# Kernel tuning notes

Hardware: AMD Instinct MI355X
Metric: run time of the kernel (lower is better)

The kernel has to match this reference:

```python
import jax, jax.numpy as jnp
import numpy as np

B, S, D = 4, 2048, 1024
H, E = 16, 64  # n_heads, head_size; H*E == D


def setup_inputs() -> dict:
    key = jax.random.key(0)
    ks = jax.random.split(key, 6)
    sd = 1.0 / np.sqrt(D)
    x = jax.random.normal(ks[0], (B, S, D), dtype=jnp.float32)
    # per-head Q/K/V projection weights, stacked: [H, D, E]
    Wq = jax.random.uniform(ks[1], (H, D, E), jnp.float32, -sd, sd)
    Wk = jax.random.uniform(ks[2], (H, D, E), jnp.float32, -sd, sd)
    Wv = jax.random.uniform(ks[3], (H, D, E), jnp.float32, -sd, sd)
    Wp = jax.random.uniform(ks[4], (D, D), jnp.float32, -sd, sd)
    bp = jax.random.uniform(ks[5], (D,), jnp.float32, -sd, sd)
    return {"x": x, "Wq": Wq, "Wk": Wk, "Wv": Wv, "Wp": Wp, "bp": bp}


def reference(x, Wq, Wk, Wv, Wp, bp):
    # Per-head projections (all heads batched): [B, H, S, E]
    q = jnp.einsum('bsd,hde->bhse', x, Wq)
    k = jnp.einsum('bsd,hde->bhse', x, Wk)
    v = jnp.einsum('bsd,hde->bhse', x, Wv)
    scale = E ** -0.5
    # Full causal score matrix [B, H, S, S]
    wei = jnp.einsum('bhse,bhte->bhst', q, k) * scale
    causal = jnp.tril(jnp.ones((S, S), dtype=bool))
    wei = jnp.where(causal, wei, -jnp.inf)
    wei = jax.nn.softmax(wei, axis=-1)
    out = jnp.einsum('bhst,bhte->bhse', wei, v)
    # concat heads along feature dim: [B, S, H*E]
    out = out.transpose(0, 2, 1, 3).reshape(B, S, H * E)
    # output projection (dropout is identity in eval)
    return out @ Wp.T + bp
```

## Files before the change

kernel.cpp:

```cpp
#include <hip/hip_runtime.h>

#define B_ 4
#define S_ 2048
#define D_ 1024
#define H_ 16
#define E_ 64
#define M_ (B_*S_)

typedef __attribute__((ext_vector_type(8))) short short8;
typedef __attribute__((ext_vector_type(4))) float floatx4;

#define GLD16(g, l) __builtin_amdgcn_global_load_lds( \
    (const __attribute__((address_space(1))) unsigned*)(g), \
    (__attribute__((address_space(3))) unsigned*)(l), 16, 0, 0)

__device__ __forceinline__ ushort f2b(float f) {
    union { float f; unsigned u; } v; v.f = f;
    unsigned r = v.u + 0x7fffu + ((v.u >> 16) & 1u);
    return (ushort)(r >> 16);
}
__device__ __forceinline__ unsigned cvt_pk_bf16(float lo, float hi) {
    unsigned r;
    asm("v_cvt_pk_bf16_f32 %0, %1, %2" : "=v"(r) : "v"(lo), "v"(hi));
    return r;
}
__device__ __forceinline__ float fast_exp2(float x) {
#if __has_builtin(__builtin_amdgcn_exp2f)
    return __builtin_amdgcn_exp2f(x);
#else
    float r; asm("v_exp_f32 %0, %1" : "=v"(r) : "v"(x)); return r;
#endif
}
__device__ __forceinline__ float lane_pull(float v, int srclane) {
    return __int_as_float(__builtin_amdgcn_ds_bpermute(srclane << 2, __float_as_int(v)));
}

__global__ __launch_bounds__(256) void cast_bf16(const float* __restrict__ in,
                                                 ushort* __restrict__ out, int n8) {
    int i = blockIdx.x * 256 + threadIdx.x;
    int stride = gridDim.x * 256;
    for (; i < n8; i += stride) {
        float4 a = ((const float4*)in)[2 * i];
        float4 b = ((const float4*)in)[2 * i + 1];
        short8 o;
        o[0] = (short)f2b(a.x); o[1] = (short)f2b(a.y);
        o[2] = (short)f2b(a.z); o[3] = (short)f2b(a.w);
        o[4] = (short)f2b(b.x); o[5] = (short)f2b(b.y);
        o[6] = (short)f2b(b.z); o[7] = (short)f2b(b.w);
        ((short8*)out)[i] = o;
    }
}

__global__ __launch_bounds__(256) void transpose_w(const float* __restrict__ Wq,
                                                   const float* __restrict__ Wk,
                                                   const float* __restrict__ Wv,
                                                   ushort* __restrict__ wt) {
    int g = blockIdx.y;
    int d0 = blockIdx.x * 64;
    const float* W = (g < 16 ? Wq : (g < 32 ? Wk : Wv)) + (size_t)(g & 15) * (D_ * E_);
    __shared__ __align__(16) ushort T[64 * 80];
    int t = threadIdx.x;
    #pragma unroll
    for (int it = 0; it < 4; ++it) {
        int i = it * 256 + t;
        int r = i >> 4, c = i & 15;
        float4 x = *(const float4*)(W + (size_t)(d0 + r) * E_ + c * 4);
        T[(c * 4 + 0) * 80 + r] = f2b(x.x);
        T[(c * 4 + 1) * 80 + r] = f2b(x.y);
        T[(c * 4 + 2) * 80 + r] = f2b(x.z);
        T[(c * 4 + 3) * 80 + r] = f2b(x.w);
    }
    __syncthreads();
    #pragma unroll
    for (int it = 0; it < 2; ++it) {
        int i = it * 256 + t;
        int e = i >> 3, c = i & 7;
        short8 x = *(const short8*)&T[e * 80 + c * 8];
        *(short8*)&wt[((size_t)g * E_ + e) * D_ + d0 + c * 8] = x;
    }
}

__global__ __launch_bounds__(256) void transpose_v(const ushort* __restrict__ v,
                                                   ushort* __restrict__ vt) {
    int s0 = blockIdx.x * 64;
    int bh = blockIdx.y;
    __shared__ __align__(16) ushort T[64 * 80];
    int t = threadIdx.x;
    #pragma unroll
    for (int it = 0; it < 2; ++it) {
        int i = it * 256 + t;
        int r = i >> 3, c = i & 7;
        short8 x = *(const short8*)&v[((size_t)bh * S_ + s0 + r) * E_ + c * 8];
        #pragma unroll
        for (int j = 0; j < 8; ++j) T[(c * 8 + j) * 80 + r] = (ushort)x[j];
    }
    __syncthreads();
    #pragma unroll
    for (int it = 0; it < 2; ++it) {
        int i = it * 256 + t;
        int e = i >> 3, c = i & 7;
        short8 x = *(const short8*)&T[e * 80 + c * 8];
        *(short8*)&vt[((size_t)bh * E_ + e) * S_ + s0 + c * 8] = x;
    }
}

__global__ __launch_bounds__(256) void gemm_qkv(const ushort* __restrict__ xb,
                                                const ushort* __restrict__ wt,
                                                ushort* __restrict__ qkv) {
    const int m0 = blockIdx.x * 256;
    const int wh = blockIdx.y;
    const ushort* Wg = wt + (size_t)wh * (E_ * D_);
    ushort* outw = qkv + (size_t)(wh >> 4) * ((size_t)B_ * H_ * S_ * E_);
    const int h = wh & 15;

    __shared__ __align__(16) ushort As[256 * 32];
    __shared__ __align__(16) ushort Bs[64 * 32];

    const int t = threadIdx.x, l = t & 63, wid = t >> 6;
    floatx4 acc[4][4] = {};

    for (int k0 = 0; k0 < D_; k0 += 32) {
        __syncthreads();
        #pragma unroll
        for (int it = 0; it < 4; ++it) {
            int i = it * 256 + t;
            int r = i >> 2, cs = i & 3;
            int c = cs ^ ((r >> 1) & 3);
            GLD16(xb + (size_t)(m0 + r) * D_ + k0 + c * 8, &As[i * 8]);
        }
        {
            int r = t >> 2, cs = t & 3;
            int c = cs ^ ((r >> 1) & 3);
            GLD16(Wg + (size_t)r * D_ + k0 + c * 8, &Bs[t * 8]);
        }
        __syncthreads();

        short8 af[4], bf[4];
        #pragma unroll
        for (int mf = 0; mf < 4; ++mf) {
            int row = wid * 64 + 16 * mf + (l & 15);
            int c = (l >> 4) ^ ((row >> 1) & 3);
            af[mf] = *(const short8*)&As[row * 32 + c * 8];
        }
        #pragma unroll
        for (int nf = 0; nf < 4; ++nf) {
            int row = 16 * nf + (l & 15);
            int c = (l >> 4) ^ ((row >> 1) & 3);
            bf[nf] = *(const short8*)&Bs[row * 32 + c * 8];
        }
        #pragma unroll
        for (int mf = 0; mf < 4; ++mf)
            #pragma unroll
            for (int nf = 0; nf < 4; ++nf)
                acc[mf][nf] = __builtin_amdgcn_mfma_f32_16x16x32_bf16(af[mf], bf[nf], acc[mf][nf], 0, 0, 0);
    }

    #pragma unroll
    for (int mf = 0; mf < 4; ++mf)
        #pragma unroll
        for (int nf = 0; nf < 4; ++nf)
            #pragma unroll
            for (int r = 0; r < 4; ++r) {
                int m = m0 + wid * 64 + 16 * mf + (l >> 4) * 4 + r;
                int b = m >> 11, s = m & (S_ - 1);
                int e = 16 * nf + (l & 15);
                outw[((size_t)((b << 4) + h) * S_ + s) * E_ + e] = f2b(acc[mf][nf][r]);
            }
}

__global__ __launch_bounds__(256) void flash(const ushort* __restrict__ qg,
                                             const ushort* __restrict__ kg,
                                             const ushort* __restrict__ vtg,
                                             ushort* __restrict__ attn) {
    const int n = blockIdx.x;
    const int x = n >> 6;
    const int bh = n & 63;
    const int b = bh >> 4, h = bh & 15;
    const ushort* qb = qg + (size_t)bh * (S_ * E_);
    const ushort* kb = kg + (size_t)bh * (S_ * E_);
    const ushort* vb = vtg + (size_t)bh * (E_ * S_);

    __shared__ __align__(16) ushort QP[64 * 64];
    __shared__ __align__(16) ushort Ks[2][64 * 64];
    __shared__ __align__(16) ushort Vs[2][64 * 64];

    const int t = threadIdx.x, l = t & 63, wid = t >> 6;
    const float SC = 0.18033688f;
    const float NEG_INF = -__builtin_inff();
    const int g = l >> 4;
    const int qloc = l & 15;
    const int qts[2] = {x, 31 - x};
    ushort* Pw = &QP[wid * 1024];

    #pragma unroll 1
    for (int qi = 0; qi < 2; ++qi) {
        const int qt = qts[qi];

        #pragma unroll
        for (int it = 0; it < 2; ++it) {
            int i = it * 256 + t;
            int r = i >> 3, cs = i & 7, c = cs ^ (r & 7);
            GLD16(qb + (size_t)(qt * 64 + r) * E_ + c * 8, &QP[i * 8]);
            GLD16(kb + (size_t)r * E_ + c * 8, &Ks[0][i * 8]);
            GLD16(vb + (size_t)r * S_ + c * 8, &Vs[0][i * 8]);
        }
        __syncthreads();

        short8 qf[2];
        #pragma unroll
        for (int ks = 0; ks < 2; ++ks) {
            int row = wid * 16 + qloc;
            int c = (g + 4 * ks) ^ (row & 7);
            qf[ks] = *(const short8*)&QP[row * 64 + c * 8];
        }

        floatx4 o[4] = {};
        float mr = NEG_INF, lr = 0.f;

        int buf = 0;
        for (int jt = 0; jt <= qt; ++jt) {
            if (jt < qt) {
                #pragma unroll
                for (int it = 0; it < 2; ++it) {
                    int i = it * 256 + t;
                    int r = i >> 3, cs = i & 7, c = cs ^ (r & 7);
                    GLD16(kb + (size_t)((jt + 1) * 64 + r) * E_ + c * 8, &Ks[buf ^ 1][i * 8]);
                    GLD16(vb + (size_t)r * S_ + (jt + 1) * 64 + c * 8, &Vs[buf ^ 1][i * 8]);
                }
            }

            floatx4 s[4] = {};
            #pragma unroll
            for (int nf = 0; nf < 4; ++nf) {
                #pragma unroll
                for (int ks = 0; ks < 2; ++ks) {
                    int row = 16 * nf + qloc;
                    int c = (g + 4 * ks) ^ (row & 7);
                    short8 kf = *(const short8*)&Ks[buf][row * 64 + c * 8];
                    s[nf] = __builtin_amdgcn_mfma_f32_16x16x32_bf16(kf, qf[ks], s[nf], 0, 0, 0);
                }
            }

            if (jt == qt) {
                int qrow = wid * 16 + qloc;
                #pragma unroll
                for (int nf = 0; nf < 4; ++nf)
                    #pragma unroll
                    for (int r = 0; r < 4; ++r)
                        if (16 * nf + 4 * g + r > qrow) s[nf][r] = NEG_INF;
            }

            float mx = s[0][0];
            #pragma unroll
            for (int nf = 0; nf < 4; ++nf)
                #pragma unroll
                for (int r = 0; r < 4; ++r) mx = fmaxf(mx, s[nf][r]);
            mx = fmaxf(mx, __shfl_xor(mx, 16));
            mx = fmaxf(mx, __shfl_xor(mx, 32));
            bool ok = (mx - mr) * SC <= 8.0f;

            if (!__all(ok)) {
                float mn = fmaxf(mr, mx);
                float al = fast_exp2((mr - mn) * SC);
                mr = mn;
                lr *= al;
                #pragma unroll
                for (int r = 0; r < 4; ++r) {
                    float alq = lane_pull(al, 4 * g + r);
                    #pragma unroll
                    for (int nf = 0; nf < 4; ++nf) o[nf][r] *= alq;
                }
            }

            {
                float nm = -mr * SC;
                float rs = 0.f;
                #pragma unroll
                for (int nf = 0; nf < 4; ++nf)
                    #pragma unroll
                    for (int r = 0; r < 4; ++r) {
                        float p = fast_exp2(fmaf(s[nf][r], SC, nm));
                        s[nf][r] = p;
                        rs += p;
                    }
                lr += rs;
            }

            #pragma unroll
            for (int nf = 0; nf < 4; ++nf) {
                unsigned pk0 = cvt_pk_bf16(s[nf][0], s[nf][1]);
                unsigned pk1 = cvt_pk_bf16(s[nf][2], s[nf][3]);
                int chunk = 2 * nf + (g >> 1);
                int sw = chunk ^ (qloc & 7);
                int a = qloc * 64 + sw * 8 + 4 * (g & 1);
                *(uint2*)&Pw[a] = make_uint2(pk0, pk1);
            }

            short8 pf[2];
            #pragma unroll
            for (int ks = 0; ks < 2; ++ks) {
                int row = l & 15;
                int c = (g + 4 * ks) ^ (row & 7);
                pf[ks] = *(const short8*)&Pw[row * 64 + c * 8];
            }
            #pragma unroll
            for (int nf = 0; nf < 4; ++nf) {
                #pragma unroll
                for (int ks = 0; ks < 2; ++ks) {
                    int row = 16 * nf + (l & 15);
                    int c = (g + 4 * ks) ^ (row & 7);
                    short8 vf = *(const short8*)&Vs[buf][row * 64 + c * 8];
                    o[nf] = __builtin_amdgcn_mfma_f32_16x16x32_bf16(pf[ks], vf, o[nf], 0, 0, 0);
                }
            }

            __syncthreads();
            buf ^= 1;
        }

        lr += __shfl_xor(lr, 16);
        lr += __shfl_xor(lr, 32);
        float inv = 1.0f / lr;
        float il[4];
        #pragma unroll
        for (int r = 0; r < 4; ++r) il[r] = lane_pull(inv, 4 * g + r);

        #pragma unroll
        for (int nf = 0; nf < 4; ++nf) {
            int col = 16 * nf + qloc;
            #pragma unroll
            for (int rp = 0; rp < 2; ++rp) {
                unsigned pk = cvt_pk_bf16(o[nf][2 * rp] * il[2 * rp],
                                          o[nf][2 * rp + 1] * il[2 * rp + 1]);
                int row0 = g * 4 + 2 * rp;
                int a0 = row0 * 64 + (((col >> 3)) ^ (row0 & 7)) * 8 + (col & 7);
                int a1 = (row0 + 1) * 64 + (((col >> 3)) ^ ((row0 + 1) & 7)) * 8 + (col & 7);
                Pw[a0] = (ushort)pk;
                Pw[a1] = (ushort)(pk >> 16);
            }
        }
        #pragma unroll
        for (int it = 0; it < 2; ++it) {
            int i = it * 64 + l;
            int row = i >> 3, cc = i & 7;
            int c = cc ^ (row & 7);
            short8 vv = *(const short8*)&Pw[row * 64 + c * 8];
            int s_abs = qt * 64 + wid * 16 + row;
            *(short8*)&attn[((size_t)(b * S_ + s_abs)) * D_ + h * E_ + cc * 8] = vv;
        }
        __syncthreads();
    }
}

__global__ __launch_bounds__(256) void out_proj(const ushort* __restrict__ a,
                                                const ushort* __restrict__ wpb,
                                                const float* __restrict__ bp,
                                                float* __restrict__ out) {
    const int m0 = blockIdx.x * 128;
    const int n0 = blockIdx.y * 128;

    __shared__ __align__(16) ushort As[128 * 32];
    __shared__ __align__(16) ushort Bs[128 * 32];

    const int t = threadIdx.x, l = t & 63, wid = t >> 6;
    const int wm = (wid & 1) * 64, wn = (wid >> 1) * 64;
    floatx4 acc[4][4] = {};

    for (int k0 = 0; k0 < D_; k0 += 32) {
        __syncthreads();
        #pragma unroll
        for (int it = 0; it < 2; ++it) {
            int i = it * 256 + t;
            int r = i >> 2, cs = i & 3;
            int c = cs ^ ((r >> 1) & 3);
            GLD16(a + (size_t)(m0 + r) * D_ + k0 + c * 8, &As[i * 8]);
            GLD16(wpb + (size_t)(n0 + r) * D_ + k0 + c * 8, &Bs[i * 8]);
        }
        __syncthreads();

        short8 af[4], bf[4];
        #pragma unroll
        for (int mf = 0; mf < 4; ++mf) {
            int row = wm + 16 * mf + (l & 15);
            int c = (l >> 4) ^ ((row >> 1) & 3);
            af[mf] = *(const short8*)&As[row * 32 + c * 8];
        }
        #pragma unroll
        for (int nf = 0; nf < 4; ++nf) {
            int row = wn + 16 * nf + (l & 15);
            int c = (l >> 4) ^ ((row >> 1) & 3);
            bf[nf] = *(const short8*)&Bs[row * 32 + c * 8];
        }
        #pragma unroll
        for (int mf = 0; mf < 4; ++mf)
            #pragma unroll
            for (int nf = 0; nf < 4; ++nf)
                acc[mf][nf] = __builtin_amdgcn_mfma_f32_16x16x32_bf16(af[mf], bf[nf], acc[mf][nf], 0, 0, 0);
    }

    #pragma unroll
    for (int nf = 0; nf < 4; ++nf) {
        int col = n0 + wn + 16 * nf + (l & 15);
        float bias = bp[col];
        #pragma unroll
        for (int mf = 0; mf < 4; ++mf)
            #pragma unroll
            for (int r = 0; r < 4; ++r) {
                int m = m0 + wm + 16 * mf + (l >> 4) * 4 + r;
                out[(size_t)m * D_ + col] = acc[mf][nf][r] + bias;
            }
    }
}

extern "C" void kernel_launch(void* const* d_in, const int* in_sizes, int n_in,
                              void* d_out, int out_size, void* d_ws, size_t ws_size,
                              hipStream_t stream) {
    const float* x  = (const float*)d_in[0];
    const float* Wq = (const float*)d_in[1];
    const float* Wk = (const float*)d_in[2];
    const float* Wv = (const float*)d_in[3];
    const float* Wp = (const float*)d_in[4];
    const float* bp = (const float*)d_in[5];

    ushort* ws = (ushort*)d_ws;
    const size_t NX  = (size_t)M_ * D_;
    const size_t NW  = (size_t)48 * E_ * D_;
    const size_t NP  = (size_t)D_ * D_;
    const size_t QSZ = (size_t)B_ * H_ * S_ * E_;
    ushort* xb    = ws;
    ushort* wt    = xb + NX;
    ushort* wpb   = wt + NW;
    ushort* qkvb  = wpb + NP;
    ushort* vt    = qkvb + 3 * QSZ;
    ushort* attnb = vt + QSZ;

    cast_bf16  <<<2048, 256, 0, stream>>>(x, xb, (int)(NX / 8));
    cast_bf16  <<<512, 256, 0, stream>>>(Wp, wpb, (int)(NP / 8));
    transpose_w<<<dim3(16, 48), 256, 0, stream>>>(Wq, Wk, Wv, wt);
    gemm_qkv   <<<dim3(M_ / 256, 48), 256, 0, stream>>>(xb, wt, qkvb);
    transpose_v<<<dim3(S_ / 64, B_ * H_), 256, 0, stream>>>(qkvb + 2 * QSZ, vt);
    flash      <<<1024, 256, 0, stream>>>(qkvb, qkvb + QSZ, vt, attnb);
    out_proj   <<<dim3(M_ / 128, D_ / 128), 256, 0, stream>>>(attnb, wpb, bp, (float*)d_out);
}
```

Before: 196.2 us.

## Fuse V transpose into QKV GEMM epilogue and widen GEMM tile to 256x128

The QKV projection GEMM now uses 512-thread blocks with a 256x128 output tile covering two heads, halving the grid in N and doubling reuse of the A tile. The V portion is written directly in transposed [b,h,e,s] layout from the MFMA accumulators using packed bf16 stores, eliminating the separate transpose_v kernel and its extra read/write of V. The transposed epilogue writes 8-byte chunks strided by S, which may be less coalesced than the row-major store.

```diff
diff --git a/kernel.cpp b/kernel.cpp
--- a/kernel.cpp
+++ b/kernel.cpp
@@ -80,50 +80,26 @@
     }
 }
 
-__global__ __launch_bounds__(256) void transpose_v(const ushort* __restrict__ v,
-                                                   ushort* __restrict__ vt) {
-    int s0 = blockIdx.x * 64;
-    int bh = blockIdx.y;
-    __shared__ __align__(16) ushort T[64 * 80];
-    int t = threadIdx.x;
-    #pragma unroll
-    for (int it = 0; it < 2; ++it) {
-        int i = it * 256 + t;
-        int r = i >> 3, c = i & 7;
-        short8 x = *(const short8*)&v[((size_t)bh * S_ + s0 + r) * E_ + c * 8];
-        #pragma unroll
-        for (int j = 0; j < 8; ++j) T[(c * 8 + j) * 80 + r] = (ushort)x[j];
-    }
-    __syncthreads();
-    #pragma unroll
-    for (int it = 0; it < 2; ++it) {
-        int i = it * 256 + t;
-        int e = i >> 3, c = i & 7;
-        short8 x = *(const short8*)&T[e * 80 + c * 8];
-        *(short8*)&vt[((size_t)bh * E_ + e) * S_ + s0 + c * 8] = x;
-    }
-}
-
-__global__ __launch_bounds__(256) void gemm_qkv(const ushort* __restrict__ xb,
+__global__ __launch_bounds__(512) void gemm_qkv(const ushort* __restrict__ xb,
                                                 const ushort* __restrict__ wt,
-                                                ushort* __restrict__ qkv) {
+                                                ushort* __restrict__ qk,
+                                                ushort* __restrict__ vt) {
     const int m0 = blockIdx.x * 256;
-    const int wh = blockIdx.y;
-    const ushort* Wg = wt + (size_t)wh * (E_ * D_);
-    ushort* outw = qkv + (size_t)(wh >> 4) * ((size_t)B_ * H_ * S_ * E_);
-    const int h = wh & 15;
+    const int n0 = blockIdx.y * 128;
+    const int w  = n0 >> 10;
 
     __shared__ __align__(16) ushort As[256 * 32];
-    __shared__ __align__(16) ushort Bs[64 * 32];
+    __shared__ __align__(16) ushort Bs[128 * 32];
 
     const int t = threadIdx.x, l = t & 63, wid = t >> 6;
+    const int wm = (wid & 3) * 64, wn = (wid >> 2) * 64;
     floatx4 acc[4][4] = {};
 
     for (int k0 = 0; k0 < D_; k0 += 32) {
         __syncthreads();
         #pragma unroll
-        for (int it = 0; it < 4; ++it) {
-            int i = it * 256 + t;
+        for (int it = 0; it < 2; ++it) {
+            int i = it * 512 + t;
             int r = i >> 2, cs = i & 3;
             int c = cs ^ ((r >> 1) & 3);
             GLD16(xb + (size_t)(m0 + r) * D_ + k0 + c * 8, &As[i * 8]);
@@ -131,20 +107,20 @@
         {
             int r = t >> 2, cs = t & 3;
             int c = cs ^ ((r >> 1) & 3);
-            GLD16(Wg + (size_t)r * D_ + k0 + c * 8, &Bs[t * 8]);
+            GLD16(wt + (size_t)(n0 + r) * D_ + k0 + c * 8, &Bs[t * 8]);
         }
         __syncthreads();
 
         short8 af[4], bf[4];
         #pragma unroll
         for (int mf = 0; mf < 4; ++mf) {
-            int row = wid * 64 + 16 * mf + (l & 15);
+            int row = wm + 16 * mf + (l & 15);
             int c = (l >> 4) ^ ((row >> 1) & 3);
             af[mf] = *(const short8*)&As[row * 32 + c * 8];
         }
         #pragma unroll
         for (int nf = 0; nf < 4; ++nf) {
-            int row = 16 * nf + (l & 15);
+            int row = wn + 16 * nf + (l & 15);
             int c = (l >> 4) ^ ((row >> 1) & 3);
             bf[nf] = *(const short8*)&Bs[row * 32 + c * 8];
         }
@@ -155,17 +131,36 @@
                 acc[mf][nf] = __builtin_amdgcn_mfma_f32_16x16x32_bf16(af[mf], bf[nf], acc[mf][nf], 0, 0, 0);
     }
 
-    #pragma unroll
-    for (int mf = 0; mf < 4; ++mf)
-        #pragma unroll
-        for (int nf = 0; nf < 4; ++nf)
-            #pragma unroll
-            for (int r = 0; r < 4; ++r) {
-                int m = m0 + wid * 64 + 16 * mf + (l >> 4) * 4 + r;
-                int b = m >> 11, s = m & (S_ - 1);
-                int e = 16 * nf + (l & 15);
-                outw[((size_t)((b << 4) + h) * S_ + s) * E_ + e] = f2b(acc[mf][nf][r]);
-            }
+    if (w < 2) {
+        ushort* outw = qk + (size_t)w * ((size_t)B_ * H_ * S_ * E_);
+        #pragma unroll
+        for (int mf = 0; mf < 4; ++mf)
+            #pragma unroll
+            for (int nf = 0; nf < 4; ++nf) {
+                int n = n0 + wn + 16 * nf + (l & 15);
+                int h = (n >> 6) & 15, e = n & 63;
+                #pragma unroll
+                for (int r = 0; r < 4; ++r) {
+                    int m = m0 + wm + 16 * mf + (l >> 4) * 4 + r;
+                    int b = m >> 11, s = m & (S_ - 1);
+                    outw[((size_t)((b << 4) + h) * S_ + s) * E_ + e] = f2b(acc[mf][nf][r]);
+                }
+            }
+    } else {
+        #pragma unroll
+        for (int mf = 0; mf < 4; ++mf) {
+            int m = m0 + wm + 16 * mf + (l >> 4) * 4;
+            int b = m >> 11, s = m & (S_ - 1);
+            #pragma unroll
+            for (int nf = 0; nf < 4; ++nf) {
+                int n = n0 + wn + 16 * nf + (l & 15);
+                int h = (n >> 6) & 15, e = n & 63;
+                unsigned pk0 = cvt_pk_bf16(acc[mf][nf][0], acc[mf][nf][1]);
+                unsigned pk1 = cvt_pk_bf16(acc[mf][nf][2], acc[mf][nf][3]);
+                *(uint2*)&vt[((size_t)((b << 4) + h) * E_ + e) * S_ + s] = make_uint2(pk0, pk1);
+            }
+        }
+    }
 }
 
 __global__ __launch_bounds__(256) void flash(const ushort* __restrict__ qg,
@@ -430,15 +425,14 @@
     ushort* xb    = ws;
     ushort* wt    = xb + NX;
     ushort* wpb   = wt + NW;
-    ushort* qkvb  = wpb + NP;
-    ushort* vt    = qkvb + 3 * QSZ;
+    ushort* qk    = wpb + NP;
+    ushort* vt    = qk + 2 * QSZ;
     ushort* attnb = vt + QSZ;
 
     cast_bf16  <<<2048, 256, 0, stream>>>(x, xb, (int)(NX / 8));
     cast_bf16  <<<512, 256, 0, stream>>>(Wp, wpb, (int)(NP / 8));
     transpose_w<<<dim3(16, 48), 256, 0, stream>>>(Wq, Wk, Wv, wt);
-    gemm_qkv   <<<dim3(M_ / 256, 48), 256, 0, stream>>>(xb, wt, qkvb);
-    transpose_v<<<dim3(S_ / 64, B_ * H_), 256, 0, stream>>>(qkvb + 2 * QSZ, vt);
-    flash      <<<1024, 256, 0, stream>>>(qkvb, qkvb + QSZ, vt, attnb);
+    gemm_qkv   <<<dim3(M_ / 256, 24), 512, 0, stream>>>(xb, wt, qk, vt);
+    flash      <<<1024, 256, 0, stream>>>(qk, qk + QSZ, vt, attnb);
     out_proj   <<<dim3(M_ / 128, D_ / 128), 256, 0, stream>>>(attnb, wpb, bp, (float*)d_out);
 }
```

Result: faster. 185.1 us (-5.7%).
